# Kernel tuning notes

Hardware: AMD Instinct MI355X
Metric: run time of the kernel (lower is better)

Reference implementation:

```python
import jax, jax.numpy as jnp
import numpy as np

K_LEN, I_LEN, DIM = 1024, 8192, 128


def setup_inputs() -> dict:
    key = jax.random.key(0)
    k1, k2 = jax.random.split(key)
    kernel = jax.random.normal(k1, (K_LEN, DIM), dtype=jnp.float32)
    x = jax.random.normal(k2, (I_LEN, DIM), dtype=jnp.float32)
    return {"kernel": kernel, "x": x}


def _cost_matrix(kernel, x):
    # squared Euclidean pairwise distances, (K, I), via GEMM form
    k2 = jnp.sum(kernel * kernel, axis=-1)  # (K,)
    x2 = jnp.sum(x * x, axis=-1)            # (I,)
    c = k2[:, None] + x2[None, :] - 2.0 * (kernel @ x.T)
    return jnp.maximum(c, 0.0)


def _acc_matrix(c):
    # DTW DP: D[i,j] = c[i,j] + min(D[i-1,j-1], D[i-1,j], D[i,j-1])
    # Row recurrence solved per-row with a (min,+) prefix scan:
    #   e[j] = min(D_prev[j-1], D_prev[j]) + c[j]   (e[0] = D_prev[0] + c[0])
    #   D[j] = S[j] + cummin(e - S),  S = cumsum(c_row)
    row0 = jnp.cumsum(c[0])

    def step(prev, c_row):
        m = jnp.concatenate([prev[:1], jnp.minimum(prev[:-1], prev[1:])])
        e = m + c_row
        S = jnp.cumsum(c_row)
        row = S + jax.lax.cummin(e - S)
        return row, row

    _, rows = jax.lax.scan(step, row0, c[1:])
    return jnp.concatenate([row0[None, :], rows], axis=0)  # (K, I)


def _backtrack(D):
    # tslearn-style backtracking from (K-1, I-1) to (0, 0).
    # Candidate order [diag, up, left]; argmin ties pick first (diag),
    # matching numpy.argmin used by tslearn. Out-of-range -> +inf border.
    K, I = D.shape
    Dp = jnp.full((K + 1, I + 1), jnp.inf, dtype=D.dtype).at[1:, 1:].set(D)
    L = K + I - 1  # max possible path length

    def step(carry, _):
        k, i, fin = carry
        emit = (k, i, jnp.logical_not(fin))
        fin2 = fin | ((k == 0) & (i == 0))
        cand = jnp.stack([Dp[k, i], Dp[k, i + 1], Dp[k + 1, i]])
        a = jnp.argmin(cand)
        nk = jnp.where(fin2, k, k - (a != 2).astype(k.dtype))
        ni = jnp.where(fin2, i, i - (a != 1).astype(i.dtype))
        return (nk, ni, fin2), emit

    init = (jnp.int32(K - 1), jnp.int32(I - 1), jnp.bool_(False))
    _, (ks, iss, valid) = jax.lax.scan(step, init, None, length=L)
    return ks, iss, valid


def reference(kernel, x):
    # Path search uses detached tensors in the original module.
    c = jax.lax.stop_gradient(_cost_matrix(kernel, x))
    D = _acc_matrix(c)
    ks, iss, valid = _backtrack(D)
    # sum of squared diffs along the optimal alignment path (gather + reduce)
    d2 = jnp.sum((kernel[ks] - x[iss]) ** 2, axis=-1)  # (L,)
    return jnp.sum(jnp.where(valid, d2, 0.0))
```

## Files before the change

### kernel.cpp

```cpp
#include <hip/hip_runtime.h>
#include <hip/hip_bf16.h>

typedef unsigned short ushort_t;
typedef unsigned int uint_t;

#define KL 1024
#define IL 8192
#define DIMV 128
#define NS 16
#define NB 258
#define NIT 269
#define SSH (8256*64)
#define GATE 416
#define INF __builtin_inff()

typedef __attribute__((ext_vector_type(8))) short v8s;
typedef __attribute__((ext_vector_type(4))) float v4f;

__global__ __launch_bounds__(256) void knorms(
    const float* __restrict__ kern, const float* __restrict__ xx,
    float* __restrict__ x2, float* __restrict__ k2, int* __restrict__ flags) {
  if (blockIdx.x == 0 && threadIdx.x < NS) flags[threadIdx.x] = 0;
  const int lane = threadIdx.x & 63;
  const int row = blockIdx.x * 4 + (threadIdx.x >> 6);
  const float* src;
  float* dst;
  if (row < IL) { src = xx + (size_t)row * DIMV; dst = x2 + row; }
  else          { src = kern + (size_t)(row - IL) * DIMV; dst = k2 + (row - IL); }
  float2 v = *(const float2*)(src + lane * 2);
  float ss = v.x * v.x + v.y * v.y;
  #pragma unroll
  for (int off = 32; off > 0; off >>= 1) ss += __shfl_down(ss, off, 64);
  if (lane == 0) *dst = ss;
}

__device__ __forceinline__ v8s pack_bf16x8(float4 a, float4 b) {
  union { unsigned int u[4]; v8s v; } r;
  union { __hip_bfloat162 h; unsigned int u; } t;
  t.h = __float22bfloat162_rn(make_float2(a.x, a.y)); r.u[0] = t.u;
  t.h = __float22bfloat162_rn(make_float2(a.z, a.w)); r.u[1] = t.u;
  t.h = __float22bfloat162_rn(make_float2(b.x, b.y)); r.u[2] = t.u;
  t.h = __float22bfloat162_rn(make_float2(b.z, b.w)); r.u[3] = t.u;
  return r.v;
}

__global__ __launch_bounds__(256) void kgemm(
    const float* __restrict__ kern, const float* __restrict__ xx,
    const float* __restrict__ x2, const float* __restrict__ k2,
    ushort_t* __restrict__ c_h) {
  __shared__ float ctile[64 * 64];
  const int T = threadIdx.x;
  const int w = T >> 6;
  const int lane = T & 63;
  const int lo = lane & 15;
  const int hi = lane >> 4;
  const int i0 = blockIdx.x * 64;
  const int s  = blockIdx.y;
  const int kr0 = s * 64;

  v4f acc[4] = {};
  #pragma unroll
  for (int ks = 0; ks < 4; ks++) {
    const int k = ks * 32 + hi * 8;
    const float* bp = xx + (size_t)(i0 + w * 16 + lo) * DIMV + k;
    v8s bf = pack_bf16x8(*(const float4*)bp, *(const float4*)(bp + 4));
    #pragma unroll
    for (int rt = 0; rt < 4; rt++) {
      const float* ap = kern + (size_t)(kr0 + rt * 16 + lo) * DIMV + k;
      v8s af = pack_bf16x8(*(const float4*)ap, *(const float4*)(ap + 4));
      acc[rt] = __builtin_amdgcn_mfma_f32_16x16x32_bf16(af, bf, acc[rt], 0, 0, 0);
    }
  }
  const float x2v = x2[i0 + w * 16 + lo];
  const int n_local = w * 16 + lo;
  #pragma unroll
  for (int rt = 0; rt < 4; rt++) {
    float4 k2f = *(const float4*)&k2[kr0 + rt * 16 + hi * 4];
    #pragma unroll
    for (int q = 0; q < 4; q++) {
      const int m_local = rt * 16 + hi * 4 + q;
      float cval = fmaxf((&k2f.x)[q] + x2v - 2.f * acc[rt][q], 0.f);
      ctile[n_local * 64 + ((m_local + 2 * n_local) & 63)] = cval;
    }
  }
  __syncthreads();
  _Float16* ob = (_Float16*)(c_h + (size_t)s * SSH);
  #pragma unroll
  for (int q = 0; q < 32; q++) {
    int tt = w + q * 4;
    int di = tt - lane;
    if (tt <= 126 && di >= 0 && di < 64) {
      int t = i0 + tt;
      ob[((size_t)(t >> 1) * 64 + lane) * 2 + (t & 1)] =
          (_Float16)ctile[di * 64 + ((lane + 2 * di) & 63)];
    }
  }
}

__device__ __forceinline__ float dpp_wave_shr1(float oldv, float src) {
  return __int_as_float(__builtin_amdgcn_update_dpp(
      __float_as_int(oldv), __float_as_int(src), 0x138, 0xF, 0xF, false));
}

__global__ __launch_bounds__(384) void kdp(
    const ushort_t* __restrict__ c_h, float* __restrict__ bound,
    int* __restrict__ flags, float* __restrict__ out) {
  __shared__ uint_t cbuf[4 * 3 * 1024];
  __shared__ __align__(16) float ring[4 * 4 * 32];
  __shared__ __align__(16) float feed[4 * 32];
  __shared__ uint_t dump[1024];
  const int g = blockIdx.x;
  const int wv = threadIdx.x >> 6;
  const int lane = threadIdx.x & 63;
  const int sb = g * 4;

  float Dcur = INF, Dul = INF;
  int fchk = 0, fpend = 0;
  float rfeed = INF;
  const float* bin = bound + (size_t)(sb > 0 ? sb - 1 : 0) * IL;
  float* bout3 = bound + (size_t)(sb + 3) * IL;

  if (wv == 4) {
    const char* gs = (const char*)(c_h + (size_t)sb * SSH);
    #pragma unroll
    for (int b = 0; b < 2; b++) {
      uint_t* dst = cbuf + b * 1024;
      #pragma unroll
      for (int q = 0; q < 4; q++)
        __builtin_amdgcn_global_load_lds(
            (const __attribute__((address_space(1))) void*)(gs + (size_t)b * 4096 + (size_t)q * 1024 + lane * 16),
            (__attribute__((address_space(3))) void*)(dst + q * 256 + lane * 4), 16, 0, 0);
    }
  } else if (wv == 5) {
    if (g > 0) {
      int f;
      do { f = __hip_atomic_load(&flags[sb - 1], __ATOMIC_RELAXED, __HIP_MEMORY_SCOPE_AGENT); } while (f < GATE);
      fchk = f; fpend = f;
      if (lane < 32) {
        feed[lane]      = __hip_atomic_load(&bin[lane],      __ATOMIC_RELAXED, __HIP_MEMORY_SCOPE_AGENT);
        feed[32 + lane] = __hip_atomic_load(&bin[32 + lane], __ATOMIC_RELAXED, __HIP_MEMORY_SCOPE_AGENT);
        rfeed           = __hip_atomic_load(&bin[64 + lane], __ATOMIC_RELAXED, __HIP_MEMORY_SCOPE_AGENT);
      }
    } else {
      if (lane < 32) { feed[lane] = INF; feed[32+lane] = INF; feed[64+lane] = INF; feed[96+lane] = INF; }
    }
  } else if (wv < 4) {
    if (g == 0 && wv == 0 && lane == 0) Dcur = 0.f;
  }
  __syncthreads();

  int s0 = 0;
  for (int i = 0; i < NIT; i++) {
    if (wv < 4) {
      const int W = i - 3 * wv;
      if (W >= 0 && W < NB) {
        const uint_t* lc = cbuf + (wv * 3 + s0) * 1024 + lane;
        uint_t lv[16];
        #pragma unroll
        for (int tp = 0; tp < 16; tp++) lv[tp] = lc[tp * 64];
        const float* fb = (wv == 0) ? &feed[(W & 3) * 32]
                                    : &ring[(wv - 1) * 128 + (W & 3) * 32];
        float fv[32];
        #pragma unroll
        for (int q = 0; q < 8; q++) {
          float4 f4 = *(const float4*)(fb + q * 4);
          fv[4 * q]     = f4.x; fv[4 * q + 1] = f4.y;
          fv[4 * q + 2] = f4.z; fv[4 * q + 3] = f4.w;
        }
        float cvv[32];
        #pragma unroll
        for (int tp = 0; tp < 16; tp++) {
          union { uint_t u; _Float16 h[2]; } cu; cu.u = lv[tp];
          cvv[2 * tp]     = (float)cu.h[0];
          cvv[2 * tp + 1] = (float)cu.h[1];
        }
        float bb[32];
        if (W >= 2 && W < 256) {
          #pragma unroll
          for (int tt = 0; tt < 32; tt++) {
            float Dup = dpp_wave_shr1(fv[tt], Dcur);
            float m1 = fminf(Dul, Dcur);
            Dcur = cvv[tt] + fminf(m1, Dup);
            Dul = Dup;
            bb[tt] = Dcur;
          }
        } else {
          const int t0 = W * 32;
          #pragma unroll
          for (int tt = 0; tt < 32; tt++) {
            const int t = t0 + tt;
            float Dup = dpp_wave_shr1(fv[tt], Dcur);
            float m1 = fminf(Dul, Dcur);
            float Dnew = cvv[tt] + fminf(m1, Dup);
            const bool alo = (t >= lane);
            const bool ahi = (t - lane < IL);
            if (alo) Dul = Dup;
            if (alo && ahi) Dcur = Dnew;
            bb[tt] = Dcur;
          }
        }
        if (lane == 63) {
          const int base2 = wv * 128 + (((W - 2) & 3) << 5);
          const int base1 = wv * 128 + (((W - 1) & 3) << 5);
          if (W >= 2) {
            #pragma unroll
            for (int tt = 0; tt < 31; tt++) ring[base2 + tt + 1] = bb[tt];
          }
          if (W >= 1) ring[base1] = bb[31];
        }
      }
      __syncthreads();
    } else if (wv == 4) {
      int ip2 = s0 + 2; if (ip2 >= 3) ip2 -= 3;
      #pragma unroll
      for (int k = 0; k < 4; k++) {
        const int B = i + 2 - 3 * k;
        const bool ok = (B >= 0 && B < NB);
        const char* src = ok
            ? ((const char*)(c_h + (size_t)(sb + k) * SSH) + (size_t)B * 4096)
            : (const char*)c_h;
        uint_t* dst = ok ? (cbuf + (k * 3 + ip2) * 1024) : dump;
        #pragma unroll
        for (int q = 0; q < 4; q++)
          __builtin_amdgcn_global_load_lds(
              (const __attribute__((address_space(1))) void*)(src + (size_t)q * 1024 + lane * 16),
              (__attribute__((address_space(3))) void*)(dst + q * 256 + lane * 4), 16, 0, 0);
      }
      asm volatile("s_waitcnt vmcnt(16)" ::: "memory");
      __builtin_amdgcn_s_barrier();
    } else {
      asm volatile("s_waitcnt vmcnt(0)" ::: "memory");
      if (g > 0) {
        if (fpend > fchk) fchk = fpend;
        const int Fw = i + 2;
        if (Fw >= 2 && Fw <= 255 && lane < 32) feed[(Fw & 3) * 32 + lane] = rfeed;
        const int Fl = i + 3;
        if (Fl <= 255) {
          const int need = 32 * (Fl + 1);
          if (fchk < need) {
            int f;
            do { f = __hip_atomic_load(&flags[sb - 1], __ATOMIC_RELAXED, __HIP_MEMORY_SCOPE_AGENT); } while (f < need);
            fchk = f;
          }
          if (lane < 32)
            rfeed = __hip_atomic_load(&bin[32 * Fl + lane], __ATOMIC_RELAXED, __HIP_MEMORY_SCOPE_AGENT);
        }
        fpend = __hip_atomic_load(&flags[sb - 1], __ATOMIC_RELAXED, __HIP_MEMORY_SCOPE_AGENT);
      }
      if (g < 3) {
        const int E = i - 12;
        if (E >= 0 && E < 256 && lane < 32) {
          float bv2 = ring[3 * 128 + (E & 3) * 32 + lane];
          __hip_atomic_store(&bout3[32 * E + lane], bv2, __ATOMIC_RELAXED, __HIP_MEMORY_SCOPE_AGENT);
        }
        const int Ep = i - 13;
        if (Ep >= 0 && Ep < 256 && lane == 0)
          __hip_atomic_store(&flags[sb + 3], 32 * Ep + 32, __ATOMIC_RELAXED, __HIP_MEMORY_SCOPE_AGENT);
      }
      asm volatile("s_waitcnt lgkmcnt(0)" ::: "memory");
      __builtin_amdgcn_s_barrier();
    }
    s0 = (s0 == 2) ? 0 : s0 + 1;
  }
  asm volatile("s_waitcnt vmcnt(0)" ::: "memory");
  if (g == 3 && wv == 3 && lane == 63) out[0] = Dcur;
}

extern "C" void kernel_launch(void* const* d_in, const int* in_sizes, int n_in,
                              void* d_out, int out_size, void* d_ws, size_t ws_size,
                              hipStream_t stream) {
  const float* kern = (const float*)d_in[0];
  const float* xx   = (const float*)d_in[1];
  char* ws = (char*)d_ws;
  const size_t OFF_X2 = (size_t)NS * SSH * 2;
  const size_t OFF_K2 = OFF_X2 + (size_t)IL * 4;
  const size_t OFF_BD = OFF_K2 + (size_t)KL * 4;
  const size_t OFF_FL = OFF_BD + (size_t)NS * IL * 4;
  ushort_t* c_h  = (ushort_t*)ws;
  float* x2    = (float*)(ws + OFF_X2);
  float* k2    = (float*)(ws + OFF_K2);
  float* bnd   = (float*)(ws + OFF_BD);
  int*   flags = (int*)(ws + OFF_FL);

  knorms<<<(IL + KL) / 4, 256, 0, stream>>>(kern, xx, x2, k2, flags);
  kgemm<<<dim3(IL / 64, NS), 256, 0, stream>>>(kern, xx, x2, k2, c_h);
  kdp<<<4, 384, 0, stream>>>(c_h, bnd, flags, (float*)d_out);
}
```

Baseline: 415.5 us.

## Load DP cost tiles straight into registers with double-buffering, drop LDS loader wave

Removes the dedicated wave that staged cost tiles into LDS with global_load_lds. Each compute wave now prefetches its next 64x32 cost block directly into registers (P/Q ping-pong). The GEMM epilogue writes the fp16 cost in a new blocked layout so each lane reads 16 contiguous words. This trades LDS staging and its waitcnt coupling for direct global-load latency that must be hidden within one iteration of the serial DP chain, and raises the cross-block gate constant.

Result: slower. 466.5 us (+12.3%).

```diff
diff --git a/kernel.cpp b/kernel.cpp
--- a/kernel.cpp
+++ b/kernel.cpp
@@ -9,9 +9,9 @@
 #define DIMV 128
 #define NS 16
 #define NB 258
-#define NIT 269
+#define NIT2 270
 #define SSH (8256*64)
-#define GATE 416
+#define GATE 672
 #define INF __builtin_inff()
 
 typedef __attribute__((ext_vector_type(8))) short v8s;
@@ -91,7 +91,8 @@
     int di = tt - lane;
     if (tt <= 126 && di >= 0 && di < 64) {
       int t = i0 + tt;
-      ob[((size_t)(t >> 1) * 64 + lane) * 2 + (t & 1)] =
+      int tp = t >> 1;
+      ob[(((size_t)(tp >> 4) * 1024) + lane * 16 + (tp & 15)) * 2 + (t & 1)] =
           (_Float16)ctile[di * 64 + ((lane + 2 * di) & 63)];
     }
   }
@@ -102,13 +103,11 @@
       __float_as_int(oldv), __float_as_int(src), 0x138, 0xF, 0xF, false));
 }
 
-__global__ __launch_bounds__(384) void kdp(
+__global__ __launch_bounds__(320) void kdp(
     const ushort_t* __restrict__ c_h, float* __restrict__ bound,
     int* __restrict__ flags, float* __restrict__ out) {
-  __shared__ uint_t cbuf[4 * 3 * 1024];
   __shared__ __align__(16) float ring[4 * 4 * 32];
   __shared__ __align__(16) float feed[4 * 32];
-  __shared__ uint_t dump[1024];
   const int g = blockIdx.x;
   const int wv = threadIdx.x >> 6;
   const int lane = threadIdx.x & 63;
@@ -120,18 +119,17 @@
   const float* bin = bound + (size_t)(sb > 0 ? sb - 1 : 0) * IL;
   float* bout3 = bound + (size_t)(sb + 3) * IL;
 
-  if (wv == 4) {
-    const char* gs = (const char*)(c_h + (size_t)sb * SSH);
-    #pragma unroll
-    for (int b = 0; b < 2; b++) {
-      uint_t* dst = cbuf + b * 1024;
-      #pragma unroll
-      for (int q = 0; q < 4; q++)
-        __builtin_amdgcn_global_load_lds(
-            (const __attribute__((address_space(1))) void*)(gs + (size_t)b * 4096 + (size_t)q * 1024 + lane * 16),
-            (__attribute__((address_space(3))) void*)(dst + q * 256 + lane * 4), 16, 0, 0);
-    }
-  } else if (wv == 5) {
+  const uint_t* cbase = (const uint_t*)c_h +
+      (size_t)(sb + (wv < 4 ? wv : 0)) * (SSH / 2) + lane * 16;
+
+  uint_t P[16], Q[16];
+
+  if (wv < 4) {
+    const uint4* sp = (const uint4*)cbase;
+    *(uint4*)&P[0] = sp[0]; *(uint4*)&P[4] = sp[1];
+    *(uint4*)&P[8] = sp[2]; *(uint4*)&P[12] = sp[3];
+    if (g == 0 && wv == 0 && lane == 0) Dcur = 0.f;
+  } else {
     if (g > 0) {
       int f;
       do { f = __hip_atomic_load(&flags[sb - 1], __ATOMIC_RELAXED, __HIP_MEMORY_SCOPE_AGENT); } while (f < GATE);
@@ -144,20 +142,19 @@
     } else {
       if (lane < 32) { feed[lane] = INF; feed[32+lane] = INF; feed[64+lane] = INF; feed[96+lane] = INF; }
     }
-  } else if (wv < 4) {
-    if (g == 0 && wv == 0 && lane == 0) Dcur = 0.f;
   }
   __syncthreads();
 
-  int s0 = 0;
-  for (int i = 0; i < NIT; i++) {
+  auto body = [&](int i, uint_t (&cur)[16], uint_t (&nxt)[16]) {
     if (wv < 4) {
       const int W = i - 3 * wv;
+      int Wn = W + 1; Wn = Wn < 0 ? 0 : (Wn > NB - 1 ? NB - 1 : Wn);
+      {
+        const uint4* sp = (const uint4*)(cbase + (size_t)Wn * 1024);
+        *(uint4*)&nxt[0]  = sp[0]; *(uint4*)&nxt[4]  = sp[1];
+        *(uint4*)&nxt[8]  = sp[2]; *(uint4*)&nxt[12] = sp[3];
+      }
       if (W >= 0 && W < NB) {
-        const uint_t* lc = cbuf + (wv * 3 + s0) * 1024 + lane;
-        uint_t lv[16];
-        #pragma unroll
-        for (int tp = 0; tp < 16; tp++) lv[tp] = lc[tp * 64];
         const float* fb = (wv == 0) ? &feed[(W & 3) * 32]
                                     : &ring[(wv - 1) * 128 + (W & 3) * 32];
         float fv[32];
@@ -170,7 +167,7 @@
         float cvv[32];
         #pragma unroll
         for (int tp = 0; tp < 16; tp++) {
-          union { uint_t u; _Float16 h[2]; } cu; cu.u = lv[tp];
+          union { uint_t u; _Float16 h[2]; } cu; cu.u = cur[tp];
           cvv[2 * tp]     = (float)cu.h[0];
           cvv[2 * tp + 1] = (float)cu.h[1];
         }
@@ -209,24 +206,7 @@
           if (W >= 1) ring[base1] = bb[31];
         }
       }
-      __syncthreads();
-    } else if (wv == 4) {
-      int ip2 = s0 + 2; if (ip2 >= 3) ip2 -= 3;
-      #pragma unroll
-      for (int k = 0; k < 4; k++) {
-        const int B = i + 2 - 3 * k;
-        const bool ok = (B >= 0 && B < NB);
-        const char* src = ok
-            ? ((const char*)(c_h + (size_t)(sb + k) * SSH) + (size_t)B * 4096)
-            : (const char*)c_h;
-        uint_t* dst = ok ? (cbuf + (k * 3 + ip2) * 1024) : dump;
-        #pragma unroll
-        for (int q = 0; q < 4; q++)
-          __builtin_amdgcn_global_load_lds(
-              (const __attribute__((address_space(1))) void*)(src + (size_t)q * 1024 + lane * 16),
-              (__attribute__((address_space(3))) void*)(dst + q * 256 + lane * 4), 16, 0, 0);
-      }
-      asm volatile("s_waitcnt vmcnt(16)" ::: "memory");
+      asm volatile("s_waitcnt lgkmcnt(0)" ::: "memory");
       __builtin_amdgcn_s_barrier();
     } else {
       asm volatile("s_waitcnt vmcnt(0)" ::: "memory");
@@ -260,8 +240,13 @@
       asm volatile("s_waitcnt lgkmcnt(0)" ::: "memory");
       __builtin_amdgcn_s_barrier();
     }
-    s0 = (s0 == 2) ? 0 : s0 + 1;
-  }
+  };
+
+  for (int i = 0; i < NIT2; i += 2) {
+    body(i, P, Q);
+    body(i + 1, Q, P);
+  }
+
   asm volatile("s_waitcnt vmcnt(0)" ::: "memory");
   if (g == 3 && wv == 3 && lane == 63) out[0] = Dcur;
 }
@@ -284,5 +269,5 @@
 
   knorms<<<(IL + KL) / 4, 256, 0, stream>>>(kern, xx, x2, k2, flags);
   kgemm<<<dim3(IL / 64, NS), 256, 0, stream>>>(kern, xx, x2, k2, c_h);
-  kdp<<<4, 384, 0, stream>>>(c_h, bnd, flags, (float*)d_out);
-}
+  kdp<<<4, 320, 0, stream>>>(c_h, bnd, flags, (float*)d_out);
+}
```
